# Optimization experiments

Hardware: AMD Instinct MI355X
Metric: run time of the kernel (lower is better)

## Reference

```python
import jax, jax.numpy as jnp
import numpy as np

N = 100000   # nodes
E = 1600000  # edges (avg degree 16)
D = 128      # feature / hidden dim
C = 64       # classes
L = 4        # number of GCNII layers
ALPHA = 0.1
LAMDA = 0.5


def setup_inputs() -> dict:
    key = jax.random.key(0)
    ks = jax.random.split(key, 8)
    stdv = 1.0 / np.sqrt(D)
    x = jax.random.normal(ks[0], (N, D), jnp.float32)
    edge_src = jax.random.randint(ks[1], (E,), 0, N)
    edge_dst = jax.random.randint(ks[2], (E,), 0, N)
    edge_weight = jax.random.uniform(ks[3], (E,), jnp.float32)
    w_in = jax.random.uniform(ks[4], (D, D), jnp.float32, -stdv, stdv)
    b_in = jnp.zeros((D,), jnp.float32)
    gcn_w = jax.random.uniform(ks[5], (L, D, D), jnp.float32, -stdv, stdv)
    w_out = jax.random.uniform(ks[6], (D, C), jnp.float32, -stdv, stdv)
    b_out = jnp.zeros((C,), jnp.float32)
    return {"x": x, "edge_src": edge_src, "edge_dst": edge_dst,
            "edge_weight": edge_weight, "w_in": w_in, "b_in": b_in,
            "gcn_w": gcn_w, "w_out": w_out, "b_out": b_out}


def _spmm(edge_src, edge_dst, edge_weight, h):
    # torch.sparse.mm(adj, h): out[i] = sum_j adj[i,j] * h[j]
    # row = dst, col = src in COO terms.
    return jax.ops.segment_sum(edge_weight[:, None] * h[edge_src],
                               edge_dst, num_segments=N)


def reference(x, edge_src, edge_dst, edge_weight, w_in, b_in, gcn_w, w_out, b_out):
    h0 = jax.nn.relu(x @ w_in + b_in)          # [N, D] initial residual
    h = h0
    for l in range(L):
        # GCNConvII called with l_arg = l+1 -> theta = log(lamda/(l_arg+1) + 1)
        theta = float(np.log(LAMDA / (l + 2) + 1.0))
        hi = _spmm(edge_src, edge_dst, edge_weight, h)      # sparse SpMM
        support = (1.0 - ALPHA) * hi + ALPHA * h0           # initial-residual mix
        out = theta * (support @ gcn_w[l]) + (1.0 - theta) * support
        out = out + h                                       # identity residual
        h = jax.nn.relu(out)
    logits = h @ w_out + b_out                              # [N, C]
    return jax.nn.log_softmax(logits, axis=1)
```

## Files before the change

kernel.cpp:

```cpp
#include <hip/hip_runtime.h>
#include <math.h>

#define N_NODES 100000
#define N_EDGES 1600000
#define DIM     128
#define NCLS    64
#define ALPHA   0.1f

#define SCAN_B  98
#define NB      391
#define NF      ((size_t)N_NODES * DIM)
#define STRIPES (N_NODES / 16)
#define CHUNK   4096

typedef __attribute__((ext_vector_type(8))) short  bf16x8;
typedef __attribute__((ext_vector_type(4))) float  f32x4;
typedef __attribute__((ext_vector_type(2))) float  f32x2;

__device__ __forceinline__ float bf2f(unsigned short u) {
    return __uint_as_float((unsigned int)u << 16);
}
__device__ __forceinline__ unsigned short f2bf(float x) {
    unsigned int u = __float_as_uint(x);
    u += 0x7FFFu + ((u >> 16) & 1u);
    return (unsigned short)(u >> 16);
}

#define BFLO(u) __uint_as_float((u) << 16)
#define BFHI(u) __uint_as_float((u) & 0xFFFF0000u)


__global__ __launch_bounds__(256) void k_hist(const int* __restrict__ dst,
                                              int* __restrict__ bucket_cnt) {
    __shared__ int hist[NB];
    int t = threadIdx.x;
    for (int b = t; b < NB; b += 256) hist[b] = 0;
    __syncthreads();
    int base = blockIdx.x * CHUNK;
    int end = min(base + CHUNK, N_EDGES);
    for (int i = base + t; i < end; i += 256)
        atomicAdd(&hist[dst[i] >> 8], 1);
    __syncthreads();
    for (int b = t; b < NB; b += 256)
        if (hist[b]) atomicAdd(&bucket_cnt[b], hist[b]);
}

__global__ __launch_bounds__(512) void k_scanb(const int* __restrict__ bucket_cnt,
                                               int* __restrict__ bucket_base,
                                               int* __restrict__ bucket_cursor) {
    __shared__ int s[512];
    int t = threadIdx.x;
    int v = (t < NB) ? bucket_cnt[t] : 0;
    s[t] = v;
    __syncthreads();
    for (int off = 1; off < 512; off <<= 1) {
        int u = (t >= off) ? s[t - off] : 0;
        __syncthreads();
        s[t] += u;
        __syncthreads();
    }
    if (t < NB) {
        int base = s[t] - v;
        bucket_base[t] = base;
        bucket_cursor[t] = base;
    }
    if (t == 0) bucket_base[NB] = N_EDGES;
}

__global__ __launch_bounds__(256) void k_part(const int* __restrict__ src,
                                              const int* __restrict__ dst,
                                              const float* __restrict__ ew,
                                              int* __restrict__ bucket_cursor,
                                              int2* __restrict__ ebuf) {
    __shared__ int lhist[NB], gbase[NB];
    int t = threadIdx.x;
    for (int b = t; b < NB; b += 256) lhist[b] = 0;
    __syncthreads();
    int base = blockIdx.x * CHUNK;
    int end = min(base + CHUNK, N_EDGES);
    for (int i = base + t; i < end; i += 256)
        atomicAdd(&lhist[dst[i] >> 8], 1);
    __syncthreads();
    for (int b = t; b < NB; b += 256) {
        int c = lhist[b];
        gbase[b] = c ? atomicAdd(&bucket_cursor[b], c) : 0;
        lhist[b] = 0;
    }
    __syncthreads();
    for (int i = base + t; i < end; i += 256) {
        int d = dst[i];
        int b = d >> 8;
        int r = atomicAdd(&lhist[b], 1);
        ebuf[gbase[b] + r] = make_int2(src[i] | ((d & 255) << 17),
                                       __float_as_int((1.0f - ALPHA) * ew[i]));
    }
}

__global__ __launch_bounds__(256) void k_deg(const int2* __restrict__ ebuf,
                                             const int* __restrict__ bucket_base,
                                             int* __restrict__ deg) {
    __shared__ int cnt[256];
    int t = threadIdx.x, b = blockIdx.x;
    cnt[t] = 0;
    __syncthreads();
    int beg = bucket_base[b], end = bucket_base[b + 1];
    for (int i = beg + t; i < end; i += 256)
        atomicAdd(&cnt[ebuf[i].x >> 17], 1);
    __syncthreads();
    int node = b * 256 + t;
    if (node < N_NODES) deg[node] = cnt[t];
}

__global__ __launch_bounds__(1024) void k_scan1(const int* __restrict__ deg,
                                                int* __restrict__ row_ptr,
                                                int* __restrict__ blocksum) {
    __shared__ int s[1024];
    int t = threadIdx.x;
    int i = blockIdx.x * 1024 + t;
    int v = (i < N_NODES) ? deg[i] : 0;
    s[t] = v;
    __syncthreads();
    for (int off = 1; off < 1024; off <<= 1) {
        int u = (t >= off) ? s[t - off] : 0;
        __syncthreads();
        s[t] += u;
        __syncthreads();
    }
    if (i < N_NODES) row_ptr[i] = s[t] - v;
    if (t == 1023) blocksum[blockIdx.x] = s[1023];
}

__global__ __launch_bounds__(128) void k_scan2(int* __restrict__ blocksum) {
    __shared__ int s[128];
    int t = threadIdx.x;
    int v = (t < SCAN_B) ? blocksum[t] : 0;
    s[t] = v;
    __syncthreads();
    for (int off = 1; off < 128; off <<= 1) {
        int u = (t >= off) ? s[t - off] : 0;
        __syncthreads();
        s[t] += u;
        __syncthreads();
    }
    if (t < SCAN_B) blocksum[t] = s[t] - v;
}

__global__ __launch_bounds__(1024) void k_scan3(int* __restrict__ row_ptr,
                                                const int* __restrict__ blocksum) {
    int t = threadIdx.x;
    int i = blockIdx.x * 1024 + t;
    if (i < N_NODES) row_ptr[i] += blocksum[blockIdx.x];
    if (i == 0) row_ptr[N_NODES] = N_EDGES;
}

__global__ __launch_bounds__(256) void k_scatter2(const int2* __restrict__ ebuf,
                                                  const int* __restrict__ bucket_base,
                                                  const int* __restrict__ row_ptr,
                                                  int2* __restrict__ colw) {
    __shared__ int lcur[256];
    int t = threadIdx.x, b = blockIdx.x;
    int node = b * 256 + t;
    lcur[t] = (node < N_NODES) ? row_ptr[node] : 0;
    __syncthreads();
    int beg = bucket_base[b], end = bucket_base[b + 1];
    for (int i = beg + t; i < end; i += 256) {
        int2 e = ebuf[i];
        int pos = atomicAdd(&lcur[e.x >> 17], 1);
        colw[pos] = make_int2(e.x & 0x1FFFF, e.y);
    }
}

__global__ void k_prepw(const float* __restrict__ gcnw, const float* __restrict__ wout,
                        const float* __restrict__ win, unsigned short* __restrict__ wp) {
    int tid = blockIdx.x * 256 + threadIdx.x;
    if (tid < 65536) {
        int l = tid >> 14;
        int r = tid & 16383;
        int j = r & 7, lane = (r >> 3) & 63, ch = (r >> 9) & 3, nt = r >> 11;
        int n = nt * 16 + (lane & 15);
        int k = ch * 32 + (lane >> 4) * 8 + j;
        wp[tid] = f2bf(gcnw[l * 16384 + k * 128 + n]);
    } else if (tid < 73728) {
        int r = tid - 65536;
        int j = r & 7, lane = (r >> 3) & 63, ch = (r >> 9) & 3, nt = r >> 11;
        int n = nt * 16 + (lane & 15);
        int k = ch * 32 + (lane >> 4) * 8 + j;
        wp[tid] = f2bf(wout[k * 64 + n]);
    } else if (tid < 90112) {
        int r = tid - 73728;
        int j = r & 7, lane = (r >> 3) & 63, ch = (r >> 9) & 3, nt = r >> 11;
        int n = nt * 16 + (lane & 15);
        int k = ch * 32 + (lane >> 4) * 8 + j;
        wp[tid] = f2bf(win[k * 128 + n]);
    }
}

#define ACC4(rr, ww) {                                        \
    f32x2 t;                                                  \
    t.x = BFLO(rr.x); t.y = BFHI(rr.x); acc2[0] += ww * t;    \
    t.x = BFLO(rr.y); t.y = BFHI(rr.y); acc2[1] += ww * t;    \
    t.x = BFLO(rr.z); t.y = BFHI(rr.z); acc2[2] += ww * t;    \
    t.x = BFLO(rr.w); t.y = BFHI(rr.w); acc2[3] += ww * t; }

__global__ __launch_bounds__(256, 8) void k_spmm_csr(
    const int* __restrict__ row_ptr, const int2* __restrict__ colw,
    const unsigned short* __restrict__ h, const unsigned short* __restrict__ h0,
    unsigned short* __restrict__ out) {
    int node = blockIdx.x * 4 + (threadIdx.x >> 6);
    if (node >= N_NODES) return;
    int lane = threadIdx.x & 63;
    int slot = lane >> 4;
    int seg  = lane & 15;
    int beg = row_ptr[node], end = row_ptr[node + 1];

    f32x2 acc2[4];
    #pragma unroll
    for (int j = 0; j < 4; j++) acc2[j] = (f32x2){0.f, 0.f};
    if (slot == 0) {
        uint4 z = *(const uint4*)(h0 + (size_t)node * DIM + seg * 8);
        acc2[0].x = ALPHA * BFLO(z.x); acc2[0].y = ALPHA * BFHI(z.x);
        acc2[1].x = ALPHA * BFLO(z.y); acc2[1].y = ALPHA * BFHI(z.y);
        acc2[2].x = ALPHA * BFLO(z.z); acc2[2].y = ALPHA * BFHI(z.z);
        acc2[3].x = ALPHA * BFLO(z.w); acc2[3].y = ALPHA * BFHI(z.w);
    }

    int last = end - 1;
    for (int e = beg; e < end; e += 16) {
        int e0 = e + slot, e1 = e0 + 4, e2 = e0 + 8, e3 = e0 + 12;
        int2 c0 = colw[min(e0, last)];
        int2 c1 = colw[min(e1, last)];
        int2 c2 = colw[min(e2, last)];
        int2 c3 = colw[min(e3, last)];
        uint4 r0 = *(const uint4*)(h + (size_t)c0.x * DIM + seg * 8);
        uint4 r1 = *(const uint4*)(h + (size_t)c1.x * DIM + seg * 8);
        uint4 r2 = *(const uint4*)(h + (size_t)c2.x * DIM + seg * 8);
        uint4 r3 = *(const uint4*)(h + (size_t)c3.x * DIM + seg * 8);
        float w0 = (e0 < end) ? __int_as_float(c0.y) : 0.f;
        float w1 = (e1 < end) ? __int_as_float(c1.y) : 0.f;
        float w2 = (e2 < end) ? __int_as_float(c2.y) : 0.f;
        float w3 = (e3 < end) ? __int_as_float(c3.y) : 0.f;
        ACC4(r0, w0);
        ACC4(r1, w1);
        ACC4(r2, w2);
        ACC4(r3, w3);
    }

    #pragma unroll
    for (int j = 0; j < 4; j++) {
        acc2[j].x += __shfl_xor(acc2[j].x, 16);
        acc2[j].y += __shfl_xor(acc2[j].y, 16);
        acc2[j].x += __shfl_xor(acc2[j].x, 32);
        acc2[j].y += __shfl_xor(acc2[j].y, 32);
    }

    if (slot == 0) {
        unsigned int p0 = (unsigned int)f2bf(acc2[0].x) | ((unsigned int)f2bf(acc2[0].y) << 16);
        unsigned int p1 = (unsigned int)f2bf(acc2[1].x) | ((unsigned int)f2bf(acc2[1].y) << 16);
        unsigned int p2 = (unsigned int)f2bf(acc2[2].x) | ((unsigned int)f2bf(acc2[2].y) << 16);
        unsigned int p3 = (unsigned int)f2bf(acc2[3].x) | ((unsigned int)f2bf(acc2[3].y) << 16);
        *(uint4*)(out + (size_t)node * DIM + seg * 8) = make_uint4(p0, p1, p2, p3);
    }
}

__global__ __launch_bounds__(256) void k_in_mfma(
    const float* __restrict__ x, const unsigned short* __restrict__ wp,
    const float* __restrict__ b_in, unsigned short* __restrict__ h0) {
    int wave = threadIdx.x >> 6, lane = threadIdx.x & 63;
    int stripe = blockIdx.x * 4 + wave;
    if (stripe >= STRIPES) return;
    int r0 = stripe * 16;
    int m = lane & 15, q = lane >> 4;

    f32x4 acc[8];
    #pragma unroll
    for (int nt = 0; nt < 8; nt++) acc[nt] = (f32x4){0.f, 0.f, 0.f, 0.f};

    const float* xr = x + (size_t)(r0 + m) * DIM + q * 8;
    #pragma unroll
    for (int ch = 0; ch < 4; ch++) {
        float4 a0 = *(const float4*)(xr + ch * 32);
        float4 a1 = *(const float4*)(xr + ch * 32 + 4);
        bf16x8 a;
        a[0] = (short)f2bf(a0.x); a[1] = (short)f2bf(a0.y);
        a[2] = (short)f2bf(a0.z); a[3] = (short)f2bf(a0.w);
        a[4] = (short)f2bf(a1.x); a[5] = (short)f2bf(a1.y);
        a[6] = (short)f2bf(a1.z); a[7] = (short)f2bf(a1.w);
        #pragma unroll
        for (int nt = 0; nt < 8; nt++) {
            bf16x8 b = *(const bf16x8*)(wp + (((nt * 4 + ch) * 64 + lane) << 3));
            acc[nt] = __builtin_amdgcn_mfma_f32_16x16x32_bf16(a, b, acc[nt], 0, 0, 0);
        }
    }

    #pragma unroll
    for (int nt = 0; nt < 8; nt++) {
        int col = nt * 16 + m;
        float bias = b_in[col];
        #pragma unroll
        for (int r = 0; r < 4; r++) {
            int row = r0 + q * 4 + r;
            h0[(size_t)row * DIM + col] = f2bf(fmaxf(acc[nt][r] + bias, 0.f));
        }
    }
}

__global__ __launch_bounds__(256) void k_layer_mfma(
    const unsigned short* __restrict__ s_in, const unsigned short* __restrict__ hprev,
    const unsigned short* __restrict__ wp, unsigned short* __restrict__ hout,
    float theta) {
    int wave = threadIdx.x >> 6, lane = threadIdx.x & 63;
    int stripe = blockIdx.x * 4 + wave;
    if (stripe >= STRIPES) return;
    int r0 = stripe * 16;
    int m = lane & 15, q = lane >> 4;
    float omt = 1.f - theta;

    f32x4 acc[8];
    #pragma unroll
    for (int nt = 0; nt < 8; nt++) acc[nt] = (f32x4){0.f, 0.f, 0.f, 0.f};

    const unsigned short* arow = s_in + (size_t)(r0 + m) * DIM + q * 8;
    #pragma unroll
    for (int ch = 0; ch < 4; ch++) {
        bf16x8 a = *(const bf16x8*)(arow + ch * 32);
        #pragma unroll
        for (int nt = 0; nt < 8; nt++) {
            bf16x8 b = *(const bf16x8*)(wp + (((nt * 4 + ch) * 64 + lane) << 3));
            acc[nt] = __builtin_amdgcn_mfma_f32_16x16x32_bf16(a, b, acc[nt], 0, 0, 0);
        }
    }

    #pragma unroll
    for (int nt = 0; nt < 8; nt++) {
        int col = nt * 16 + m;
        #pragma unroll
        for (int r = 0; r < 4; r++) {
            int row = r0 + q * 4 + r;
            size_t idx = (size_t)row * DIM + col;
            float sup = bf2f(s_in[idx]);
            float hp  = bf2f(hprev[idx]);
            float o = theta * acc[nt][r] + omt * sup + hp;
            hout[idx] = f2bf(fmaxf(o, 0.f));
        }
    }
}

__global__ __launch_bounds__(256) void k_out_mfma(
    const unsigned short* __restrict__ h, const unsigned short* __restrict__ wp,
    const float* __restrict__ bo, float* __restrict__ out) {
    int wave = threadIdx.x >> 6, lane = threadIdx.x & 63;
    int stripe = blockIdx.x * 4 + wave;
    if (stripe >= STRIPES) return;
    int r0 = stripe * 16;
    int m = lane & 15, q = lane >> 4;

    f32x4 acc[4];
    #pragma unroll
    for (int nt = 0; nt < 4; nt++) acc[nt] = (f32x4){0.f, 0.f, 0.f, 0.f};

    const unsigned short* arow = h + (size_t)(r0 + m) * DIM + q * 8;
    #pragma unroll
    for (int ch = 0; ch < 4; ch++) {
        bf16x8 a = *(const bf16x8*)(arow + ch * 32);
        #pragma unroll
        for (int nt = 0; nt < 4; nt++) {
            bf16x8 b = *(const bf16x8*)(wp + (((nt * 4 + ch) * 64 + lane) << 3));
            acc[nt] = __builtin_amdgcn_mfma_f32_16x16x32_bf16(a, b, acc[nt], 0, 0, 0);
        }
    }

    float v[4][4];
    #pragma unroll
    for (int nt = 0; nt < 4; nt++) {
        float bias = bo[nt * 16 + m];
        #pragma unroll
        for (int r = 0; r < 4; r++) v[nt][r] = acc[nt][r] + bias;
    }
    #pragma unroll
    for (int r = 0; r < 4; r++) {
        float mx = fmaxf(fmaxf(v[0][r], v[1][r]), fmaxf(v[2][r], v[3][r]));
        #pragma unroll
        for (int off = 1; off < 16; off <<= 1) mx = fmaxf(mx, __shfl_xor(mx, off));
        float s = 0.f;
        #pragma unroll
        for (int nt = 0; nt < 4; nt++) s += __expf(v[nt][r] - mx);
        #pragma unroll
        for (int off = 1; off < 16; off <<= 1) s += __shfl_xor(s, off);
        float lse = mx + logf(s);
        int row = r0 + q * 4 + r;
        #pragma unroll
        for (int nt = 0; nt < 4; nt++)
            out[(size_t)row * NCLS + nt * 16 + m] = v[nt][r] - lse;
    }
}

extern "C" void kernel_launch(void* const* d_in, const int* in_sizes, int n_in,
                              void* d_out, int out_size, void* d_ws, size_t ws_size,
                              hipStream_t stream) {
    const float* x    = (const float*)d_in[0];
    const int*   esrc = (const int*)d_in[1];
    const int*   edst = (const int*)d_in[2];
    const float* ew   = (const float*)d_in[3];
    const float* w_in = (const float*)d_in[4];
    const float* b_in = (const float*)d_in[5];
    const float* gcnw = (const float*)d_in[6];
    const float* wout = (const float*)d_in[7];
    const float* bout = (const float*)d_in[8];
    float* out = (float*)d_out;

    unsigned short* h0 = (unsigned short*)d_ws;
    unsigned short* hA = h0 + NF;
    unsigned short* hB = hA + NF;
    unsigned short* hi = hB + NF;
    unsigned short* wp = hi + NF;
    int2* colw = (int2*)(wp + 90112);
    int2* ebuf = colw + N_EDGES;
    int*  row_ptr       = (int*)(ebuf + N_EDGES);
    int*  deg           = row_ptr + (N_NODES + 1);
    int*  blocksum      = deg + N_NODES;
    int*  bucket_cnt    = blocksum + SCAN_B;
    int*  bucket_base   = bucket_cnt + NB;
    int*  bucket_cursor = bucket_base + (NB + 1);

    const int PART_B = (N_EDGES + CHUNK - 1) / CHUNK;
    const int MFMA_BLOCKS = (STRIPES + 3) / 4;

    k_prepw<<<(90112 + 255) / 256, 256, 0, stream>>>(gcnw, wout, w_in, wp);

    hipMemsetAsync(bucket_cnt, 0, NB * sizeof(int), stream);
    k_hist<<<PART_B, 256, 0, stream>>>(edst, bucket_cnt);
    k_scanb<<<1, 512, 0, stream>>>(bucket_cnt, bucket_base, bucket_cursor);
    k_part<<<PART_B, 256, 0, stream>>>(esrc, edst, ew, bucket_cursor, ebuf);
    k_deg<<<NB, 256, 0, stream>>>(ebuf, bucket_base, deg);
    k_scan1<<<SCAN_B, 1024, 0, stream>>>(deg, row_ptr, blocksum);
    k_scan2<<<1, 128, 0, stream>>>(blocksum);
    k_scan3<<<SCAN_B, 1024, 0, stream>>>(row_ptr, blocksum);
    k_scatter2<<<NB, 256, 0, stream>>>(ebuf, bucket_base, row_ptr, colw);

    k_in_mfma<<<MFMA_BLOCKS, 256, 0, stream>>>(x, wp + 73728, b_in, h0);

    const unsigned short* hprev = h0;
    unsigned short* bufs[2] = {hA, hB};
    for (int l = 0; l < 4; l++) {
        float theta = logf(0.5f / (float)(l + 2) + 1.0f);
        k_spmm_csr<<<(N_NODES + 3) / 4, 256, 0, stream>>>(row_ptr, colw, hprev, h0, hi);
        unsigned short* hnew = bufs[l & 1];
        k_layer_mfma<<<MFMA_BLOCKS, 256, 0, stream>>>(hi, hprev, wp + (size_t)l * 16384,
                                                      hnew, theta);
        hprev = hnew;
    }

    k_out_mfma<<<MFMA_BLOCKS, 256, 0, stream>>>(hprev, wp + 65536, bout, out);
}
```

Measured before the change: 556.4 us.

## Switch activations and weights from bf16 to fp16 with packed half2 SpMM accumulation

Every stored activation and weight moves from bf16 to fp16. The SpMM now accumulates in packed half2 FMAs instead of unpacking to fp32, and the edge weights are pre-duplicated into a half2 at CSR build time. The intent is to cut the ALU cost of the gather-accumulate loop (conversions and scalar FMAs) and to drop the bf16 round-to-nearest conversion code. The cost is lower accumulation precision and fp16 range limits in the SpMM reductions, which could affect accuracy.

Measured after the change: 551.7 us. About the same (-0.8%).

```diff
diff --git a/kernel.cpp b/kernel.cpp
--- a/kernel.cpp
+++ b/kernel.cpp
@@ -1,4 +1,5 @@
 #include <hip/hip_runtime.h>
+#include <hip/hip_fp16.h>
 #include <math.h>
 
 #define N_NODES 100000
@@ -13,21 +14,15 @@
 #define STRIPES (N_NODES / 16)
 #define CHUNK   4096
 
-typedef __attribute__((ext_vector_type(8))) short  bf16x8;
-typedef __attribute__((ext_vector_type(4))) float  f32x4;
-typedef __attribute__((ext_vector_type(2))) float  f32x2;
-
-__device__ __forceinline__ float bf2f(unsigned short u) {
-    return __uint_as_float((unsigned int)u << 16);
-}
-__device__ __forceinline__ unsigned short f2bf(float x) {
-    unsigned int u = __float_as_uint(x);
-    u += 0x7FFFu + ((u >> 16) & 1u);
-    return (unsigned short)(u >> 16);
-}
-
-#define BFLO(u) __uint_as_float((u) << 16)
-#define BFHI(u) __uint_as_float((u) & 0xFFFF0000u)
+typedef __attribute__((ext_vector_type(8))) _Float16 f16x8;
+typedef __attribute__((ext_vector_type(4))) float    f32x4;
+
+__device__ __forceinline__ __half2 u2h2(unsigned int u) {
+    union { unsigned int u; __half2 h; } x; x.u = u; return x.h;
+}
+__device__ __forceinline__ unsigned int h22u(__half2 h) {
+    union { unsigned int u; __half2 h; } x; x.h = h; return x.u;
+}
 
 
 __global__ __launch_bounds__(256) void k_hist(const int* __restrict__ dst,
@@ -166,7 +161,8 @@
     for (int i = beg + t; i < end; i += 256) {
         int2 e = ebuf[i];
         int pos = atomicAdd(&lcur[e.x >> 17], 1);
-        colw[pos] = make_int2(e.x & 0x1FFFF, e.y);
+        unsigned int w2 = h22u(__float2half2_rn(__int_as_float(e.y)));
+        colw[pos] = make_int2(e.x & 0x1FFFF, (int)w2);
     }
 }
 
@@ -179,28 +175,21 @@
         int j = r & 7, lane = (r >> 3) & 63, ch = (r >> 9) & 3, nt = r >> 11;
         int n = nt * 16 + (lane & 15);
         int k = ch * 32 + (lane >> 4) * 8 + j;
-        wp[tid] = f2bf(gcnw[l * 16384 + k * 128 + n]);
+        wp[tid] = __half_as_ushort(__float2half(gcnw[l * 16384 + k * 128 + n]));
     } else if (tid < 73728) {
         int r = tid - 65536;
         int j = r & 7, lane = (r >> 3) & 63, ch = (r >> 9) & 3, nt = r >> 11;
         int n = nt * 16 + (lane & 15);
         int k = ch * 32 + (lane >> 4) * 8 + j;
-        wp[tid] = f2bf(wout[k * 64 + n]);
+        wp[tid] = __half_as_ushort(__float2half(wout[k * 64 + n]));
     } else if (tid < 90112) {
         int r = tid - 73728;
         int j = r & 7, lane = (r >> 3) & 63, ch = (r >> 9) & 3, nt = r >> 11;
         int n = nt * 16 + (lane & 15);
         int k = ch * 32 + (lane >> 4) * 8 + j;
-        wp[tid] = f2bf(win[k * 128 + n]);
-    }
-}
-
-#define ACC4(rr, ww) {                                        \
-    f32x2 t;                                                  \
-    t.x = BFLO(rr.x); t.y = BFHI(rr.x); acc2[0] += ww * t;    \
-    t.x = BFLO(rr.y); t.y = BFHI(rr.y); acc2[1] += ww * t;    \
-    t.x = BFLO(rr.z); t.y = BFHI(rr.z); acc2[2] += ww * t;    \
-    t.x = BFLO(rr.w); t.y = BFHI(rr.w); acc2[3] += ww * t; }
+        wp[tid] = __half_as_ushort(__float2half(win[k * 128 + n]));
+    }
+}
 
 __global__ __launch_bounds__(256, 8) void k_spmm_csr(
     const int* __restrict__ row_ptr, const int2* __restrict__ colw,
@@ -213,15 +202,15 @@
     int seg  = lane & 15;
     int beg = row_ptr[node], end = row_ptr[node + 1];
 
-    f32x2 acc2[4];
-    #pragma unroll
-    for (int j = 0; j < 4; j++) acc2[j] = (f32x2){0.f, 0.f};
+    __half2 z2 = __float2half2_rn(0.f);
+    __half2 acc2[4] = {z2, z2, z2, z2};
     if (slot == 0) {
         uint4 z = *(const uint4*)(h0 + (size_t)node * DIM + seg * 8);
-        acc2[0].x = ALPHA * BFLO(z.x); acc2[0].y = ALPHA * BFHI(z.x);
-        acc2[1].x = ALPHA * BFLO(z.y); acc2[1].y = ALPHA * BFHI(z.y);
-        acc2[2].x = ALPHA * BFLO(z.z); acc2[2].y = ALPHA * BFHI(z.z);
-        acc2[3].x = ALPHA * BFLO(z.w); acc2[3].y = ALPHA * BFHI(z.w);
+        __half2 al2 = __float2half2_rn(ALPHA);
+        acc2[0] = __hmul2(al2, u2h2(z.x));
+        acc2[1] = __hmul2(al2, u2h2(z.y));
+        acc2[2] = __hmul2(al2, u2h2(z.z));
+        acc2[3] = __hmul2(al2, u2h2(z.w));
     }
 
     int last = end - 1;
@@ -235,30 +224,39 @@
         uint4 r1 = *(const uint4*)(h + (size_t)c1.x * DIM + seg * 8);
         uint4 r2 = *(const uint4*)(h + (size_t)c2.x * DIM + seg * 8);
         uint4 r3 = *(const uint4*)(h + (size_t)c3.x * DIM + seg * 8);
-        float w0 = (e0 < end) ? __int_as_float(c0.y) : 0.f;
-        float w1 = (e1 < end) ? __int_as_float(c1.y) : 0.f;
-        float w2 = (e2 < end) ? __int_as_float(c2.y) : 0.f;
-        float w3 = (e3 < end) ? __int_as_float(c3.y) : 0.f;
-        ACC4(r0, w0);
-        ACC4(r1, w1);
-        ACC4(r2, w2);
-        ACC4(r3, w3);
+        __half2 w0 = (e0 < end) ? u2h2((unsigned int)c0.y) : z2;
+        __half2 w1 = (e1 < end) ? u2h2((unsigned int)c1.y) : z2;
+        __half2 w2 = (e2 < end) ? u2h2((unsigned int)c2.y) : z2;
+        __half2 w3 = (e3 < end) ? u2h2((unsigned int)c3.y) : z2;
+        acc2[0] = __hfma2(w0, u2h2(r0.x), acc2[0]);
+        acc2[1] = __hfma2(w0, u2h2(r0.y), acc2[1]);
+        acc2[2] = __hfma2(w0, u2h2(r0.z), acc2[2]);
+        acc2[3] = __hfma2(w0, u2h2(r0.w), acc2[3]);
+        acc2[0] = __hfma2(w1, u2h2(r1.x), acc2[0]);
+        acc2[1] = __hfma2(w1, u2h2(r1.y), acc2[1]);
+        acc2[2] = __hfma2(w1, u2h2(r1.z), acc2[2]);
+        acc2[3] = __hfma2(w1, u2h2(r1.w), acc2[3]);
+        acc2[0] = __hfma2(w2, u2h2(r2.x), acc2[0]);
+        acc2[1] = __hfma2(w2, u2h2(r2.y), acc2[1]);
+        acc2[2] = __hfma2(w2, u2h2(r2.z), acc2[2]);
+        acc2[3] = __hfma2(w2, u2h2(r2.w), acc2[3]);
+        acc2[0] = __hfma2(w3, u2h2(r3.x), acc2[0]);
+        acc2[1] = __hfma2(w3, u2h2(r3.y), acc2[1]);
+        acc2[2] = __hfma2(w3, u2h2(r3.z), acc2[2]);
+        acc2[3] = __hfma2(w3, u2h2(r3.w), acc2[3]);
     }
 
     #pragma unroll
     for (int j = 0; j < 4; j++) {
-        acc2[j].x += __shfl_xor(acc2[j].x, 16);
-        acc2[j].y += __shfl_xor(acc2[j].y, 16);
-        acc2[j].x += __shfl_xor(acc2[j].x, 32);
-        acc2[j].y += __shfl_xor(acc2[j].y, 32);
+        unsigned int u = __shfl_xor(h22u(acc2[j]), 16);
+        acc2[j] = __hadd2(acc2[j], u2h2(u));
+        u = __shfl_xor(h22u(acc2[j]), 32);
+        acc2[j] = __hadd2(acc2[j], u2h2(u));
     }
 
     if (slot == 0) {
-        unsigned int p0 = (unsigned int)f2bf(acc2[0].x) | ((unsigned int)f2bf(acc2[0].y) << 16);
-        unsigned int p1 = (unsigned int)f2bf(acc2[1].x) | ((unsigned int)f2bf(acc2[1].y) << 16);
-        unsigned int p2 = (unsigned int)f2bf(acc2[2].x) | ((unsigned int)f2bf(acc2[2].y) << 16);
-        unsigned int p3 = (unsigned int)f2bf(acc2[3].x) | ((unsigned int)f2bf(acc2[3].y) << 16);
-        *(uint4*)(out + (size_t)node * DIM + seg * 8) = make_uint4(p0, p1, p2, p3);
+        *(uint4*)(out + (size_t)node * DIM + seg * 8) =
+            make_uint4(h22u(acc2[0]), h22u(acc2[1]), h22u(acc2[2]), h22u(acc2[3]));
     }
 }
 
@@ -280,15 +278,15 @@
     for (int ch = 0; ch < 4; ch++) {
         float4 a0 = *(const float4*)(xr + ch * 32);
         float4 a1 = *(const float4*)(xr + ch * 32 + 4);
-        bf16x8 a;
-        a[0] = (short)f2bf(a0.x); a[1] = (short)f2bf(a0.y);
-        a[2] = (short)f2bf(a0.z); a[3] = (short)f2bf(a0.w);
-        a[4] = (short)f2bf(a1.x); a[5] = (short)f2bf(a1.y);
-        a[6] = (short)f2bf(a1.z); a[7] = (short)f2bf(a1.w);
+        f16x8 a;
+        a[0] = (_Float16)a0.x; a[1] = (_Float16)a0.y;
+        a[2] = (_Float16)a0.z; a[3] = (_Float16)a0.w;
+        a[4] = (_Float16)a1.x; a[5] = (_Float16)a1.y;
+        a[6] = (_Float16)a1.z; a[7] = (_Float16)a1.w;
         #pragma unroll
         for (int nt = 0; nt < 8; nt++) {
-            bf16x8 b = *(const bf16x8*)(wp + (((nt * 4 + ch) * 64 + lane) << 3));
-            acc[nt] = __builtin_amdgcn_mfma_f32_16x16x32_bf16(a, b, acc[nt], 0, 0, 0);
+            f16x8 b = *(const f16x8*)(wp + (((nt * 4 + ch) * 64 + lane) << 3));
+            acc[nt] = __builtin_amdgcn_mfma_f32_16x16x32_f16(a, b, acc[nt], 0, 0, 0);
         }
     }
 
@@ -299,7 +297,8 @@
         #pragma unroll
         for (int r = 0; r < 4; r++) {
             int row = r0 + q * 4 + r;
-            h0[(size_t)row * DIM + col] = f2bf(fmaxf(acc[nt][r] + bias, 0.f));
+            h0[(size_t)row * DIM + col] =
+                __half_as_ushort(__float2half(fmaxf(acc[nt][r] + bias, 0.f)));
         }
     }
 }
@@ -322,11 +321,11 @@
     const unsigned short* arow = s_in + (size_t)(r0 + m) * DIM + q * 8;
     #pragma unroll
     for (int ch = 0; ch < 4; ch++) {
-        bf16x8 a = *(const bf16x8*)(arow + ch * 32);
+        f16x8 a = *(const f16x8*)(arow + ch * 32);
         #pragma unroll
         for (int nt = 0; nt < 8; nt++) {
-            bf16x8 b = *(const bf16x8*)(wp + (((nt * 4 + ch) * 64 + lane) << 3));
-            acc[nt] = __builtin_amdgcn_mfma_f32_16x16x32_bf16(a, b, acc[nt], 0, 0, 0);
+            f16x8 b = *(const f16x8*)(wp + (((nt * 4 + ch) * 64 + lane) << 3));
+            acc[nt] = __builtin_amdgcn_mfma_f32_16x16x32_f16(a, b, acc[nt], 0, 0, 0);
         }
     }
 
@@ -337,10 +336,10 @@
         for (int r = 0; r < 4; r++) {
             int row = r0 + q * 4 + r;
             size_t idx = (size_t)row * DIM + col;
-            float sup = bf2f(s_in[idx]);
-            float hp  = bf2f(hprev[idx]);
+            float sup = __half2float(__ushort_as_half(s_in[idx]));
+            float hp  = __half2float(__ushort_as_half(hprev[idx]));
             float o = theta * acc[nt][r] + omt * sup + hp;
-            hout[idx] = f2bf(fmaxf(o, 0.f));
+            hout[idx] = __half_as_ushort(__float2half(fmaxf(o, 0.f)));
         }
     }
 }
@@ -361,11 +360,11 @@
     const unsigned short* arow = h + (size_t)(r0 + m) * DIM + q * 8;
     #pragma unroll
     for (int ch = 0; ch < 4; ch++) {
-        bf16x8 a = *(const bf16x8*)(arow + ch * 32);
+        f16x8 a = *(const f16x8*)(arow + ch * 32);
         #pragma unroll
         for (int nt = 0; nt < 4; nt++) {
-            bf16x8 b = *(const bf16x8*)(wp + (((nt * 4 + ch) * 64 + lane) << 3));
-            acc[nt] = __builtin_amdgcn_mfma_f32_16x16x32_bf16(a, b, acc[nt], 0, 0, 0);
+            f16x8 b = *(const f16x8*)(wp + (((nt * 4 + ch) * 64 + lane) << 3));
+            acc[nt] = __builtin_amdgcn_mfma_f32_16x16x32_f16(a, b, acc[nt], 0, 0, 0);
         }
     }
 
```
